# Kernel tuning notes

Hardware: AMD Instinct MI355X
Metric: run time of the kernel (lower is better)

## Reference

```python
import math
import jax, jax.numpy as jnp
import numpy as np

B, S, D = 4, 2048, 1280
H, HD = 16, 80  # num_heads, head_dim
LOG2E = 1.442695041


def setup_inputs() -> dict:
    key = jax.random.key(0)
    ks = jax.random.split(key, 6)
    hidden_states = jax.random.normal(ks[0], (B, S, D), dtype=jnp.float32)
    # additive causal mask: 0 on/below diagonal, large negative above
    causal = jnp.tril(jnp.ones((S, S), dtype=bool))
    attention_mask = jnp.where(causal, 0.0, -1e9).astype(jnp.float32)[None, None, :, :]
    attention_mask = jnp.broadcast_to(attention_mask, (B, 1, S, S))
    scaling = jax.random.normal(ks[1], (HD,), dtype=jnp.float32)
    fan = 1.0 / math.sqrt(D)
    qkv_w = jax.random.normal(ks[2], (3 * H * HD, D), dtype=jnp.float32) * fan
    qkv_b = jax.random.normal(ks[3], (3 * H * HD,), dtype=jnp.float32) * fan
    o_w = jax.random.normal(ks[4], (D, H * HD), dtype=jnp.float32) * (1.0 / math.sqrt(H * HD))
    o_b = jax.random.normal(ks[5], (D,), dtype=jnp.float32) * fan
    return {
        "hidden_states": hidden_states,
        "attention_mask": attention_mask,
        "scaling": scaling,
        "qkv_w": qkv_w,
        "qkv_b": qkv_b,
        "o_w": o_w,
        "o_b": o_b,
    }


def reference(hidden_states, attention_mask, scaling, qkv_w, qkv_b, o_w, o_b):
    b, s, _ = hidden_states.shape
    qkv = hidden_states @ qkv_w.T + qkv_b  # [b, s, 3*H*HD]
    xq, xk, xv = jnp.split(qkv, [H * HD, 2 * H * HD], axis=-1)
    xq = xq.reshape(b, s, H, HD)
    xk = xk.reshape(b, s, H, HD)
    xv = xv.reshape(b, s, H, HD)
    # per-dim query scaling: softplus(scaling) * log2(e) / sqrt(head_dim)
    scale = jax.nn.softplus(scaling) * (LOG2E / math.sqrt(HD))
    xq = xq * scale[None, None, None, :]
    scores = jnp.einsum("bqhd,bkhd->bhqk", xq, xk) + attention_mask  # [b,H,s,s]
    probs = jax.nn.softmax(scores.astype(jnp.float32), axis=-1).astype(xq.dtype)
    out = jnp.einsum("bhqk,bkhd->bqhd", probs, xv).reshape(b, s, H * HD)
    return out @ o_w.T + o_b
```

## Files before the change

kernel.cpp:

```cpp
#include <hip/hip_runtime.h>
#include <math.h>

#define B_ 4
#define S_ 2048
#define D_ 1280
#define H_ 16
#define HD_ 80
#define HHD (H_ * HD_)
#define QKVN (3 * H_ * HD_)

typedef __bf16 bf16x8 __attribute__((ext_vector_type(8)));
typedef __bf16 bf16x4 __attribute__((ext_vector_type(4)));
typedef float  f32x4  __attribute__((ext_vector_type(4)));

__global__ __launch_bounds__(256) void cvt_bf16(
    const float* __restrict__ in, __bf16* __restrict__ out, int n8)
{
    const int i = blockIdx.x * 256 + threadIdx.x;
    if (i < n8) {
        const float4 a = ((const float4*)in)[2 * (size_t)i];
        const float4 b = ((const float4*)in)[2 * (size_t)i + 1];
        bf16x8 v = {(__bf16)a.x, (__bf16)a.y, (__bf16)a.z, (__bf16)a.w,
                    (__bf16)b.x, (__bf16)b.y, (__bf16)b.z, (__bf16)b.w};
        *(bf16x8*)(out + 8 * (size_t)i) = v;
    }
}

__device__ __forceinline__ void async_copy16(const void* g, void* l)
{
    __builtin_amdgcn_global_load_lds(
        (const __attribute__((address_space(1))) unsigned int*)g,
        (__attribute__((address_space(3))) unsigned int*)l, 16, 0, 0);
}

__device__ __forceinline__ void stage128x64(
    const __bf16* __restrict__ src, int K, char* lds, int tid)
{
    const int wave = tid >> 6, lane = tid & 63;
#pragma unroll
    for (int i = 0; i < 4; ++i) {
        const int c = (wave * 4 + i) * 64 + lane;
        const int r = c >> 3;
        const int g = (c & 7) ^ (r & 7);
        async_copy16(src + (size_t)r * K + g * 8, lds + (wave * 4 + i) * 1024);
    }
}

__device__ __forceinline__ bf16x8 frag_ld(const char* lds, int m, int j)
{
    return *(const bf16x8*)(lds + m * 128 + ((j ^ (m & 7)) << 4));
}

__device__ __forceinline__ void mfma_loop(
    const __bf16* __restrict__ A, const __bf16* __restrict__ W, int K,
    char* ldsA, char* ldsB, int tid, f32x4 acc[4][4])
{
    const int wave = tid >> 6;
    const int wm = wave >> 1, wn = wave & 1;
    const int l16 = tid & 15, quad = (tid & 63) >> 4;

#pragma unroll
    for (int mi = 0; mi < 4; ++mi)
#pragma unroll
        for (int ni = 0; ni < 4; ++ni) acc[mi][ni] = (f32x4){0.f, 0.f, 0.f, 0.f};

    for (int k0 = 0; k0 < K; k0 += 64) {
        __syncthreads();
        stage128x64(A + k0, K, ldsA, tid);
        stage128x64(W + k0, K, ldsB, tid);
        __syncthreads();
#pragma unroll
        for (int ks = 0; ks < 2; ++ks) {
            bf16x8 af[4], bfr[4];
#pragma unroll
            for (int mi = 0; mi < 4; ++mi)
                af[mi] = frag_ld(ldsA, wm * 64 + mi * 16 + l16, ks * 4 + quad);
#pragma unroll
            for (int ni = 0; ni < 4; ++ni)
                bfr[ni] = frag_ld(ldsB, wn * 64 + ni * 16 + l16, ks * 4 + quad);
#pragma unroll
            for (int mi = 0; mi < 4; ++mi)
#pragma unroll
                for (int ni = 0; ni < 4; ++ni)
                    acc[mi][ni] = __builtin_amdgcn_mfma_f32_16x16x32_bf16(
                        af[mi], bfr[ni], acc[mi][ni], 0, 0, 0);
        }
    }
}

__global__ __launch_bounds__(256) void gemm_qkv_mfma(
    const __bf16* __restrict__ Ab, const __bf16* __restrict__ Wb,
    const float* __restrict__ bias, const float* __restrict__ scaling,
    __bf16* __restrict__ Qb, __bf16* __restrict__ Kb, __bf16* __restrict__ Vtb)
{
    __shared__ __align__(16) char ldsA[128 * 128];
    __shared__ __align__(16) char ldsB[128 * 128];
    const int tid = threadIdx.x;

    const int flat = blockIdx.x;
    const int xcd = flat & 7;
    const int idx = flat >> 3;
    const int g = idx / 24;
    const int r24 = idx - g * 24;
    const int nn = r24 >> 3;
    const int mm = r24 & 7;
    const int m0 = (xcd * 8 + mm) * 128;
    const int n0 = (g * 3 + nn) * 128;

    f32x4 acc[4][4];
    mfma_loop(Ab + (size_t)m0 * D_, Wb + (size_t)n0 * D_, D_, ldsA, ldsB, tid, acc);

    const int wave = tid >> 6, wm = wave >> 1, wn = wave & 1;
    const int l16 = tid & 15, quad = (tid & 63) >> 4;
    const int sec = n0 / HHD;

    if (sec == 2) {
#pragma unroll
        for (int ni = 0; ni < 4; ++ni) {
            const int col = n0 + wn * 64 + ni * 16 + l16;
            const int cis = col - 2 * HHD;
            const int h = cis / HD_;
            const int d = cis - h * HD_;
            const float bv = bias[col];
#pragma unroll
            for (int mi = 0; mi < 4; ++mi) {
                const int row0 = m0 + wm * 64 + mi * 16 + quad * 4;
                const int bb = row0 >> 11;
                const int s = row0 & (S_ - 1);
                const size_t bh = (size_t)(bb * H_ + h);
                bf16x4 pv = {(__bf16)(acc[mi][ni][0] + bv),
                             (__bf16)(acc[mi][ni][1] + bv),
                             (__bf16)(acc[mi][ni][2] + bv),
                             (__bf16)(acc[mi][ni][3] + bv)};
                *(bf16x4*)(Vtb + (bh * HD_ + d) * S_ + s) = pv;
            }
        }
    } else {
#pragma unroll
        for (int ni = 0; ni < 4; ++ni) {
            const int col = n0 + wn * 64 + ni * 16 + l16;
            const int cis = col - sec * HHD;
            const int h = cis / HD_;
            const int d = cis - h * HD_;
            const float bv = bias[col];
            float qsv = 0.f;
            if (sec == 0)
                qsv = log1pf(expf(scaling[d])) *
                      (1.442695041f * 1.442695041f / 8.944271910f);
#pragma unroll
            for (int mi = 0; mi < 4; ++mi) {
#pragma unroll
                for (int r = 0; r < 4; ++r) {
                    const int row = m0 + wm * 64 + mi * 16 + quad * 4 + r;
                    const int bb = row >> 11;
                    const int s = row & (S_ - 1);
                    const size_t bh = (size_t)(bb * H_ + h);
                    const float v = acc[mi][ni][r] + bv;
                    if (sec == 0) Qb[(bh * S_ + s) * HD_ + d] = (__bf16)(v * qsv);
                    else          Kb[(bh * S_ + s) * HD_ + d] = (__bf16)v;
                }
            }
        }
    }
}

__global__ __launch_bounds__(256) void gemm_o_mfma(
    const __bf16* __restrict__ Ab, const __bf16* __restrict__ Wb,
    const float* __restrict__ bias, float* __restrict__ C)
{
    __shared__ __align__(16) char ldsA[128 * 128];
    __shared__ __align__(16) char ldsB[128 * 128];
    const int tid = threadIdx.x;

    const int flat = blockIdx.x;
    const int xcd = flat & 7;
    const int idx = flat >> 3;
    const int mm = idx / 10;
    const int nn = idx - mm * 10;
    const int m0 = (xcd * 8 + mm) * 128;
    const int n0 = nn * 128;

    f32x4 acc[4][4];
    mfma_loop(Ab + (size_t)m0 * D_, Wb + (size_t)n0 * D_, D_, ldsA, ldsB, tid, acc);

    const int wave = tid >> 6, wm = wave >> 1, wn = wave & 1;
    const int l16 = tid & 15, quad = (tid & 63) >> 4;

#pragma unroll
    for (int ni = 0; ni < 4; ++ni) {
        const int col = n0 + wn * 64 + ni * 16 + l16;
        const float bv = bias[col];
#pragma unroll
        for (int mi = 0; mi < 4; ++mi) {
#pragma unroll
            for (int r = 0; r < 4; ++r) {
                const int row = m0 + wm * 64 + mi * 16 + quad * 4 + r;
                C[(size_t)row * D_ + col] = acc[mi][ni][r] + bv;
            }
        }
    }
}

struct KF8 { bf16x8 f0, f1, f2; };

__device__ __forceinline__ void kload8(
    const __bf16* __restrict__ base, int row, int quad, KF8& kf)
{
    const __bf16* r = base + (size_t)row * HD_;
    kf.f0 = *(const bf16x8*)(r + quad * 8);
    kf.f1 = *(const bf16x8*)(r + 32 + quad * 8);
    bf16x8 z = {};
    if (quad < 2) z = *(const bf16x8*)(r + 64 + quad * 8);
    kf.f2 = z;
}

#define QK3(SREG, KF, QF)                                                      \
    SREG = __builtin_amdgcn_mfma_f32_16x16x32_bf16(KF.f0, QF.f0, SREG, 0, 0, 0); \
    SREG = __builtin_amdgcn_mfma_f32_16x16x32_bf16(KF.f1, QF.f1, SREG, 0, 0, 0); \
    SREG = __builtin_amdgcn_mfma_f32_16x16x32_bf16(KF.f2, QF.f2, SREG, 0, 0, 0);

#define MASK4(SREG, BASE, Q)                                                   \
    _Pragma("unroll")                                                          \
    for (int i = 0; i < 4; ++i)                                                \
        SREG[i] = ((BASE) + quad * 4 + i <= (Q) + l16) ? SREG[i] : -1e30f;

#define ATTN_BODY64(KT)                                                        \
    {                                                                          \
        const int k0 = (KT) * 64;                                              \
        const bool do_lo = ((KT) < nkt_lo);                  \
         \
        const bf16x8 vf00 = *(const bf16x8*)(Vbase + (size_t)( 0 + l16) * S_ + k0 + quad * 8);      \
        const bf16x8 vf01 = *(const bf16x8*)(Vbase + (size_t)( 0 + l16) * S_ + k0 + 32 + quad * 8); \
        const bf16x8 vf10 = *(const bf16x8*)(Vbase + (size_t)(16 + l16) * S_ + k0 + quad * 8);      \
        const bf16x8 vf11 = *(const bf16x8*)(Vbase + (size_t)(16 + l16) * S_ + k0 + 32 + quad * 8); \
        const bf16x8 vf20 = *(const bf16x8*)(Vbase + (size_t)(32 + l16) * S_ + k0 + quad * 8);      \
        const bf16x8 vf21 = *(const bf16x8*)(Vbase + (size_t)(32 + l16) * S_ + k0 + 32 + quad * 8); \
        const bf16x8 vf30 = *(const bf16x8*)(Vbase + (size_t)(48 + l16) * S_ + k0 + quad * 8);      \
        const bf16x8 vf31 = *(const bf16x8*)(Vbase + (size_t)(48 + l16) * S_ + k0 + 32 + quad * 8); \
        const bf16x8 vf40 = *(const bf16x8*)(Vbase + (size_t)(64 + l16) * S_ + k0 + quad * 8);      \
        const bf16x8 vf41 = *(const bf16x8*)(Vbase + (size_t)(64 + l16) * S_ + k0 + 32 + quad * 8); \
                          \
        f32x4 sH0 = (f32x4){0.f,0.f,0.f,0.f}, sH1 = sH0, sH2 = sH0, sH3 = sH0; \
        f32x4 sL0 = sH0, sL1 = sH0, sL2 = sH0, sL3 = sH0;                      \
        __builtin_amdgcn_s_setprio(1);                                         \
        QK3(sH0, kf0, qfH) QK3(sH1, kf1, qfH) QK3(sH2, kf2, qfH) QK3(sH3, kf3, qfH) \
        if (do_lo) {                                                           \
            QK3(sL0, kf0, qfL) QK3(sL1, kf1, qfL)                              \
            QK3(sL2, kf2, qfL) QK3(sL3, kf3, qfL)                              \
        }                                                                      \
        __builtin_amdgcn_s_setprio(0);                                         \
         \
         \
        {                                                                      \
            const int kn = ((KT) + 1 < nkt_hi ? (KT) + 1 : (KT)) * 64;         \
            kload8(Kbase, kn + l16, quad, kf0);                                \
            kload8(Kbase, kn + 16 + l16, quad, kf1);                           \
            kload8(Kbase, kn + 32 + l16, quad, kf2);                           \
            kload8(Kbase, kn + 48 + l16, quad, kf3);                           \
        }                                                                      \
                \
        float aH;                                                              \
        {                                                                      \
            if (k0 + 63 > q_hi) {                                              \
                MASK4(sH0, k0, q_hi)      MASK4(sH1, k0 + 16, q_hi)            \
                MASK4(sH2, k0 + 32, q_hi) MASK4(sH3, k0 + 48, q_hi)            \
            }                                                                  \
            float mA = fmaxf(fmaxf(sH0[0], sH0[1]), fmaxf(sH0[2], sH0[3]));    \
            float mB = fmaxf(fmaxf(sH1[0], sH1[1]), fmaxf(sH1[2], sH1[3]));    \
            float mC = fmaxf(fmaxf(sH2[0], sH2[1]), fmaxf(sH2[2], sH2[3]));    \
            float mD = fmaxf(fmaxf(sH3[0], sH3[1]), fmaxf(sH3[2], sH3[3]));    \
            float mx = fmaxf(fmaxf(mA, mB), fmaxf(mC, mD));                    \
            mx = fmaxf(mx, __shfl_xor(mx, 16));                                \
            mx = fmaxf(mx, __shfl_xor(mx, 32));                                \
            const float mn = fmaxf(mH, mx);                                    \
            aH = exp2f(mH - mn);                                               \
            mH = mn;                                                           \
            float rs = 0.f;                                                    \
            _Pragma("unroll")                                                  \
            for (int i = 0; i < 4; ++i) {                                      \
                const float p0 = exp2f(sH0[i] - mn);                           \
                const float p1 = exp2f(sH1[i] - mn);                           \
                const float p2 = exp2f(sH2[i] - mn);                           \
                const float p3 = exp2f(sH3[i] - mn);                           \
                sH0[i] = p0; sH1[i] = p1; sH2[i] = p2; sH3[i] = p3;            \
                rs += (p0 + p1) + (p2 + p3);                                   \
            }                                                                  \
            lH = lH * aH + rs;                           \
            *(bf16x4*)&Ps[wave][0][l16][0][quad * 4] =                         \
                (bf16x4){(__bf16)sH0[0], (__bf16)sH0[1], (__bf16)sH0[2], (__bf16)sH0[3]}; \
            *(bf16x4*)&Ps[wave][0][l16][0][16 + quad * 4] =                    \
                (bf16x4){(__bf16)sH1[0], (__bf16)sH1[1], (__bf16)sH1[2], (__bf16)sH1[3]}; \
            *(bf16x4*)&Ps[wave][0][l16][1][quad * 4] =                         \
                (bf16x4){(__bf16)sH2[0], (__bf16)sH2[1], (__bf16)sH2[2], (__bf16)sH2[3]}; \
            *(bf16x4*)&Ps[wave][0][l16][1][16 + quad * 4] =                    \
                (bf16x4){(__bf16)sH3[0], (__bf16)sH3[1], (__bf16)sH3[2], (__bf16)sH3[3]}; \
        }                                                                      \
                                          \
        float aL = 1.f;                                                        \
        if (do_lo) {                                                           \
            if (k0 + 63 > q_lo) {                                              \
                MASK4(sL0, k0, q_lo)      MASK4(sL1, k0 + 16, q_lo)            \
                MASK4(sL2, k0 + 32, q_lo) MASK4(sL3, k0 + 48, q_lo)            \
            }                                                                  \
            float mA = fmaxf(fmaxf(sL0[0], sL0[1]), fmaxf(sL0[2], sL0[3]));    \
            float mB = fmaxf(fmaxf(sL1[0], sL1[1]), fmaxf(sL1[2], sL1[3]));    \
            float mC = fmaxf(fmaxf(sL2[0], sL2[1]), fmaxf(sL2[2], sL2[3]));    \
            float mD = fmaxf(fmaxf(sL3[0], sL3[1]), fmaxf(sL3[2], sL3[3]));    \
            float mx = fmaxf(fmaxf(mA, mB), fmaxf(mC, mD));                    \
            mx = fmaxf(mx, __shfl_xor(mx, 16));                                \
            mx = fmaxf(mx, __shfl_xor(mx, 32));                                \
            const float mn = fmaxf(mL, mx);                                    \
            aL = exp2f(mL - mn);                                               \
            mL = mn;                                                           \
            float rs = 0.f;                                                    \
            _Pragma("unroll")                                                  \
            for (int i = 0; i < 4; ++i) {                                      \
                const float p0 = exp2f(sL0[i] - mn);                           \
                const float p1 = exp2f(sL1[i] - mn);                           \
                const float p2 = exp2f(sL2[i] - mn);                           \
                const float p3 = exp2f(sL3[i] - mn);                           \
                sL0[i] = p0; sL1[i] = p1; sL2[i] = p2; sL3[i] = p3;            \
                rs += (p0 + p1) + (p2 + p3);                                   \
            }                                                                  \
            lL = lL * aL + rs;                                                 \
            *(bf16x4*)&Ps[wave][1][l16][0][quad * 4] =                         \
                (bf16x4){(__bf16)sL0[0], (__bf16)sL0[1], (__bf16)sL0[2], (__bf16)sL0[3]}; \
            *(bf16x4*)&Ps[wave][1][l16][0][16 + quad * 4] =                    \
                (bf16x4){(__bf16)sL1[0], (__bf16)sL1[1], (__bf16)sL1[2], (__bf16)sL1[3]}; \
            *(bf16x4*)&Ps[wave][1][l16][1][quad * 4] =                         \
                (bf16x4){(__bf16)sL2[0], (__bf16)sL2[1], (__bf16)sL2[2], (__bf16)sL2[3]}; \
            *(bf16x4*)&Ps[wave][1][l16][1][16 + quad * 4] =                    \
                (bf16x4){(__bf16)sL3[0], (__bf16)sL3[1], (__bf16)sL3[2], (__bf16)sL3[3]}; \
        }                                                                      \
        asm volatile("s_waitcnt lgkmcnt(0)" ::: "memory");                     \
        const bf16x8 pfH0 = *(const bf16x8*)&Ps[wave][0][l16][0][quad * 8];    \
        const bf16x8 pfH1 = *(const bf16x8*)&Ps[wave][0][l16][1][quad * 8];    \
        const bf16x8 pfL0 = *(const bf16x8*)&Ps[wave][1][l16][0][quad * 8];    \
        const bf16x8 pfL1 = *(const bf16x8*)&Ps[wave][1][l16][1][quad * 8];    \
         \
        __builtin_amdgcn_s_setprio(1);                                         \
        {                                                                      \
            f32x4 c0, c1, c2, c3, c4;                                          \
            _Pragma("unroll")                                                  \
            for (int i = 0; i < 4; ++i) {                                      \
                c0[i] = oH0[i] * aH; c1[i] = oH1[i] * aH; c2[i] = oH2[i] * aH; \
                c3[i] = oH3[i] * aH; c4[i] = oH4[i] * aH;                      \
            }                                                                  \
            oH0 = __builtin_amdgcn_mfma_f32_16x16x32_bf16(vf00, pfH0, c0, 0, 0, 0); \
            oH1 = __builtin_amdgcn_mfma_f32_16x16x32_bf16(vf10, pfH0, c1, 0, 0, 0); \
            oH2 = __builtin_amdgcn_mfma_f32_16x16x32_bf16(vf20, pfH0, c2, 0, 0, 0); \
            oH3 = __builtin_amdgcn_mfma_f32_16x16x32_bf16(vf30, pfH0, c3, 0, 0, 0); \
            oH4 = __builtin_amdgcn_mfma_f32_16x16x32_bf16(vf40, pfH0, c4, 0, 0, 0); \
            oH0 = __builtin_amdgcn_mfma_f32_16x16x32_bf16(vf01, pfH1, oH0, 0, 0, 0); \
            oH1 = __builtin_amdgcn_mfma_f32_16x16x32_bf16(vf11, pfH1, oH1, 0, 0, 0); \
            oH2 = __builtin_amdgcn_mfma_f32_16x16x32_bf16(vf21, pfH1, oH2, 0, 0, 0); \
            oH3 = __builtin_amdgcn_mfma_f32_16x16x32_bf16(vf31, pfH1, oH3, 0, 0, 0); \
            oH4 = __builtin_amdgcn_mfma_f32_16x16x32_bf16(vf41, pfH1, oH4, 0, 0, 0); \
        }                                                                      \
        if (do_lo) {                                                           \
            f32x4 c0, c1, c2, c3, c4;                                          \
            _Pragma("unroll")                                                  \
            for (int i = 0; i < 4; ++i) {                                      \
                c0[i] = oL0[i] * aL; c1[i] = oL1[i] * aL; c2[i] = oL2[i] * aL; \
                c3[i] = oL3[i] * aL; c4[i] = oL4[i] * aL;                      \
            }                                                                  \
            oL0 = __builtin_amdgcn_mfma_f32_16x16x32_bf16(vf00, pfL0, c0, 0, 0, 0); \
            oL1 = __builtin_amdgcn_mfma_f32_16x16x32_bf16(vf10, pfL0, c1, 0, 0, 0); \
            oL2 = __builtin_amdgcn_mfma_f32_16x16x32_bf16(vf20, pfL0, c2, 0, 0, 0); \
            oL3 = __builtin_amdgcn_mfma_f32_16x16x32_bf16(vf30, pfL0, c3, 0, 0, 0); \
            oL4 = __builtin_amdgcn_mfma_f32_16x16x32_bf16(vf40, pfL0, c4, 0, 0, 0); \
            oL0 = __builtin_amdgcn_mfma_f32_16x16x32_bf16(vf01, pfL1, oL0, 0, 0, 0); \
            oL1 = __builtin_amdgcn_mfma_f32_16x16x32_bf16(vf11, pfL1, oL1, 0, 0, 0); \
            oL2 = __builtin_amdgcn_mfma_f32_16x16x32_bf16(vf21, pfL1, oL2, 0, 0, 0); \
            oL3 = __builtin_amdgcn_mfma_f32_16x16x32_bf16(vf31, pfL1, oL3, 0, 0, 0); \
            oL4 = __builtin_amdgcn_mfma_f32_16x16x32_bf16(vf41, pfL1, oL4, 0, 0, 0); \
        }                                                                      \
        __builtin_amdgcn_s_setprio(0);                                         \
    }

__global__ __launch_bounds__(256, 2) void attn_v13(
    const __bf16* __restrict__ Qb, const __bf16* __restrict__ Kb,
    const __bf16* __restrict__ Vtb, __bf16* __restrict__ out)
{
    __shared__ __align__(16) __bf16 Ps[4][2][16][2][40];

    const int tid = threadIdx.x;
    const int wave = tid >> 6;
    const int lane = tid & 63;
    const int l16 = lane & 15;
    const int quad = lane >> 4;

    const int flat = blockIdx.x;
    const int c = flat & 7;
    const int slot = flat >> 3;
    const int bhgrp = slot >> 4;
    const int xslot = slot & 15;
    const int bh = bhgrp * 8 + c;
    const int x = (xslot + 5 * bhgrp) & 15;
    const int b = bh >> 4, h = bh & 15;

    const int q_lo = 64 * x + 16 * wave;
    const int q_hi = 64 * (31 - x) + 16 * wave;

    const __bf16* Qbase = Qb + (size_t)bh * S_ * HD_;
    const __bf16* Kbase = Kb + (size_t)bh * S_ * HD_;
    const __bf16* Vbase = Vtb + (size_t)bh * HD_ * S_;

    KF8 qfL, qfH;
    kload8(Qbase, q_lo + l16, quad, qfL);
    kload8(Qbase, q_hi + l16, quad, qfH);

    float mL = -1e30f, lL = 0.f, mH = -1e30f, lH = 0.f;
    f32x4 oH0 = (f32x4){0.f,0.f,0.f,0.f}, oH1 = oH0, oH2 = oH0, oH3 = oH0, oH4 = oH0;
    f32x4 oL0 = oH0, oL1 = oH0, oL2 = oH0, oL3 = oH0, oL4 = oH0;

    const int nkt_lo = (q_lo + 16 + 63) >> 6;
    const int nkt_hi = (q_hi + 16 + 63) >> 6;

    KF8 kf0, kf1, kf2, kf3;
    kload8(Kbase, l16, quad, kf0);
    kload8(Kbase, 16 + l16, quad, kf1);
    kload8(Kbase, 32 + l16, quad, kf2);
    kload8(Kbase, 48 + l16, quad, kf3);

    for (int kt = 0; kt < nkt_hi; ++kt) {
        ATTN_BODY64(kt);
    }

    float lHs = lH + __shfl_xor(lH, 16);
    lHs += __shfl_xor(lHs, 32);
    float lLs = lL + __shfl_xor(lL, 16);
    lLs += __shfl_xor(lLs, 32);
    const float invH = 1.f / lHs;
    const float invL = 1.f / lLs;
    const size_t rowH = ((size_t)b * S_ + q_hi + l16) * HHD + h * HD_ + quad * 4;
    const size_t rowL = ((size_t)b * S_ + q_lo + l16) * HHD + h * HD_ + quad * 4;
    {
        bf16x4 v0 = {(__bf16)(oH0[0]*invH), (__bf16)(oH0[1]*invH), (__bf16)(oH0[2]*invH), (__bf16)(oH0[3]*invH)};
        bf16x4 v1 = {(__bf16)(oH1[0]*invH), (__bf16)(oH1[1]*invH), (__bf16)(oH1[2]*invH), (__bf16)(oH1[3]*invH)};
        bf16x4 v2 = {(__bf16)(oH2[0]*invH), (__bf16)(oH2[1]*invH), (__bf16)(oH2[2]*invH), (__bf16)(oH2[3]*invH)};
        bf16x4 v3 = {(__bf16)(oH3[0]*invH), (__bf16)(oH3[1]*invH), (__bf16)(oH3[2]*invH), (__bf16)(oH3[3]*invH)};
        bf16x4 v4 = {(__bf16)(oH4[0]*invH), (__bf16)(oH4[1]*invH), (__bf16)(oH4[2]*invH), (__bf16)(oH4[3]*invH)};
        *(bf16x4*)(out + rowH)      = v0;
        *(bf16x4*)(out + rowH + 16) = v1;
        *(bf16x4*)(out + rowH + 32) = v2;
        *(bf16x4*)(out + rowH + 48) = v3;
        *(bf16x4*)(out + rowH + 64) = v4;
    }
    {
        bf16x4 v0 = {(__bf16)(oL0[0]*invL), (__bf16)(oL0[1]*invL), (__bf16)(oL0[2]*invL), (__bf16)(oL0[3]*invL)};
        bf16x4 v1 = {(__bf16)(oL1[0]*invL), (__bf16)(oL1[1]*invL), (__bf16)(oL1[2]*invL), (__bf16)(oL1[3]*invL)};
        bf16x4 v2 = {(__bf16)(oL2[0]*invL), (__bf16)(oL2[1]*invL), (__bf16)(oL2[2]*invL), (__bf16)(oL2[3]*invL)};
        bf16x4 v3 = {(__bf16)(oL3[0]*invL), (__bf16)(oL3[1]*invL), (__bf16)(oL3[2]*invL), (__bf16)(oL3[3]*invL)};
        bf16x4 v4 = {(__bf16)(oL4[0]*invL), (__bf16)(oL4[1]*invL), (__bf16)(oL4[2]*invL), (__bf16)(oL4[3]*invL)};
        *(bf16x4*)(out + rowL)      = v0;
        *(bf16x4*)(out + rowL + 16) = v1;
        *(bf16x4*)(out + rowL + 32) = v2;
        *(bf16x4*)(out + rowL + 48) = v3;
        *(bf16x4*)(out + rowL + 64) = v4;
    }
}

extern "C" void kernel_launch(void* const* d_in, const int* in_sizes, int n_in,
                              void* d_out, int out_size, void* d_ws, size_t ws_size,
                              hipStream_t stream)
{
    const float* hidden  = (const float*)d_in[0];
    const float* scaling = (const float*)d_in[2];
    const float* qkv_w   = (const float*)d_in[3];
    const float* qkv_b   = (const float*)d_in[4];
    const float* o_w     = (const float*)d_in[5];
    const float* o_b     = (const float*)d_in[6];
    float* out = (float*)d_out;

    const size_t N_HID = (size_t)B_ * S_ * D_;
    const size_t N_QW  = (size_t)QKVN * D_;
    const size_t N_OW  = (size_t)D_ * D_;
    const size_t NPH   = (size_t)B_ * H_ * S_ * HD_;

    __bf16* Ab    = (__bf16*)d_ws;
    __bf16* Wqb   = Ab + N_HID;
    __bf16* Wob   = Wqb + N_QW;
    __bf16* Qb    = Wob + N_OW;
    __bf16* Kb    = Qb + NPH;
    __bf16* Vtb   = Kb + NPH;
    __bf16* attnb = Vtb + NPH;

    dim3 blk(256);

    cvt_bf16<<<dim3(N_HID / 8 / 256), blk, 0, stream>>>(hidden, Ab, N_HID / 8);
    cvt_bf16<<<dim3(N_QW  / 8 / 256), blk, 0, stream>>>(qkv_w, Wqb, N_QW / 8);
    cvt_bf16<<<dim3(N_OW  / 8 / 256), blk, 0, stream>>>(o_w,   Wob, N_OW / 8);

    gemm_qkv_mfma<<<dim3(QKVN / 128 * (B_ * S_ / 128)), blk, 0, stream>>>(
        Ab, Wqb, qkv_b, scaling, Qb, Kb, Vtb);

    attn_v13<<<dim3(16 * H_ * B_), blk, 0, stream>>>(Qb, Kb, Vtb, attnb);

    gemm_o_mfma<<<dim3(D_ / 128 * (B_ * S_ / 128)), blk, 0, stream>>>(
        attnb, Wob, o_b, out);
}
```

Baseline: 476.6 us.

## Replace QKV GEMM with 256x256-tile, 512-thread double-buffered pipelined kernel

Replaces the 128x128-tile QKV projection GEMM with a 256x256-tile kernel that uses 8 waves. It double-buffers LDS and interleaves async staging of the next K-slice with MFMA work on the current one. Larger tiles cut global and LDS traffic per FLOP, and the staged prefetch hides load latency. In exchange it needs 128KB of LDS and many accumulator registers per block, which limits occupancy. With only 480 blocks there is also a risk of poor wave balance across CUs.

New measurement: 463.2 us. 2.8% less time.

```diff
diff --git a/kernel.cpp b/kernel.cpp
--- a/kernel.cpp
+++ b/kernel.cpp
@@ -88,32 +88,111 @@
     }
 }
 
-__global__ __launch_bounds__(256) void gemm_qkv_mfma(
+__device__ __forceinline__ void stage_half256(
+    const __bf16* __restrict__ src, int K, char* ldsmat, int half, int tid)
+{
+    const int wave = tid >> 6, lane = tid & 63;
+#pragma unroll
+    for (int i = 0; i < 2; ++i) {
+        const int c = (i * 8 + wave) * 64 + lane;
+        const int r = half * 128 + (c >> 3);
+        const int g = (c & 7) ^ (r & 7);
+        async_copy16(src + (size_t)r * K + g * 8,
+                     ldsmat + half * 16384 + (i * 8 + wave) * 1024);
+    }
+}
+
+#define QBAR() do { asm volatile("" ::: "memory");                             \
+                    __builtin_amdgcn_s_barrier();                              \
+                    __builtin_amdgcn_sched_barrier(0); } while (0)
+
+__global__ __launch_bounds__(512, 2) void gemm_qkv_256(
     const __bf16* __restrict__ Ab, const __bf16* __restrict__ Wb,
     const float* __restrict__ bias, const float* __restrict__ scaling,
     __bf16* __restrict__ Qb, __bf16* __restrict__ Kb, __bf16* __restrict__ Vtb)
 {
-    __shared__ __align__(16) char ldsA[128 * 128];
-    __shared__ __align__(16) char ldsB[128 * 128];
+    __shared__ __align__(16) char lds[2][2][32768];
     const int tid = threadIdx.x;
+    const int wave = tid >> 6;
+    const int wm = wave >> 2, wn = wave & 3;
+    const int l16 = tid & 15, quad = (tid & 63) >> 4;
 
     const int flat = blockIdx.x;
     const int xcd = flat & 7;
     const int idx = flat >> 3;
-    const int g = idx / 24;
-    const int r24 = idx - g * 24;
-    const int nn = r24 >> 3;
-    const int mm = r24 & 7;
-    const int m0 = (xcd * 8 + mm) * 128;
-    const int n0 = (g * 3 + nn) * 128;
-
-    f32x4 acc[4][4];
-    mfma_loop(Ab + (size_t)m0 * D_, Wb + (size_t)n0 * D_, D_, ldsA, ldsB, tid, acc);
-
-    const int wave = tid >> 6, wm = wave >> 1, wn = wave & 1;
-    const int l16 = tid & 15, quad = (tid & 63) >> 4;
-    const int sec = n0 / HHD;
-
+    const int m_i = idx & 3, n_g = idx >> 2;
+    const int m0 = (xcd * 4 + m_i) * 256;
+    const int n0 = n_g * 256;
+
+    const __bf16* A = Ab + (size_t)m0 * D_;
+    const __bf16* W = Wb + (size_t)n0 * D_;
+
+    f32x4 acc[8][4];
+#pragma unroll
+    for (int mi = 0; mi < 8; ++mi)
+#pragma unroll
+        for (int ni = 0; ni < 4; ++ni) acc[mi][ni] = (f32x4){0.f, 0.f, 0.f, 0.f};
+
+    stage_half256(A, D_, lds[0][0], 0, tid);
+    stage_half256(A, D_, lds[0][0], 1, tid);
+    stage_half256(W, D_, lds[0][1], 0, tid);
+    stage_half256(W, D_, lds[0][1], 1, tid);
+
+    const int nt = D_ / 64;
+    bf16x8 af[4][2], bfr[2][2];
+
+#define RD_A(MH)                                                               \
+    _Pragma("unroll")                                                          \
+    for (int mi = 0; mi < 4; ++mi)                                             \
+        _Pragma("unroll")                                                      \
+        for (int ks = 0; ks < 2; ++ks)                                         \
+            af[mi][ks] = frag_ld(lA, wm * 128 + (MH) * 64 + mi * 16 + l16,     \
+                                 ks * 4 + quad);
+#define RD_B(NH)                                                               \
+    _Pragma("unroll")                                                          \
+    for (int ni = 0; ni < 2; ++ni)                                             \
+        _Pragma("unroll")                                                      \
+        for (int ks = 0; ks < 2; ++ks)                                         \
+            bfr[ni][ks] = frag_ld(lB, wn * 64 + (NH) * 32 + ni * 16 + l16,     \
+                                  ks * 4 + quad);
+#define MM16(MH, NH)                                                           \
+    __builtin_amdgcn_s_setprio(1);                                             \
+    _Pragma("unroll")                                                          \
+    for (int mi = 0; mi < 4; ++mi)                                             \
+        _Pragma("unroll")                                                      \
+        for (int ni = 0; ni < 2; ++ni) {                                       \
+            acc[(MH)*4+mi][(NH)*2+ni] = __builtin_amdgcn_mfma_f32_16x16x32_bf16( \
+                af[mi][0], bfr[ni][0], acc[(MH)*4+mi][(NH)*2+ni], 0, 0, 0);    \
+            acc[(MH)*4+mi][(NH)*2+ni] = __builtin_amdgcn_mfma_f32_16x16x32_bf16( \
+                af[mi][1], bfr[ni][1], acc[(MH)*4+mi][(NH)*2+ni], 0, 0, 0);    \
+        }                                                                      \
+    __builtin_amdgcn_s_setprio(0);
+
+    for (int t = 0; t < nt; ++t) {
+        const int cur = t & 1;
+        const char* lA = lds[cur][0];
+        const char* lB = lds[cur][1];
+        char* sA = lds[cur ^ 1][0];
+        char* sB = lds[cur ^ 1][1];
+        const int kn = (t + 1 < nt ? t + 1 : t) * 64;
+
+        stage_half256(A + kn, D_, sA, 0, tid);
+        asm volatile("s_waitcnt vmcnt(2)" ::: "memory");
+        QBAR();
+        RD_A(0) RD_B(0) MM16(0, 0)
+        stage_half256(A + kn, D_, sA, 1, tid);
+        RD_B(1) MM16(0, 1)
+        stage_half256(W + kn, D_, sB, 0, tid);
+        RD_A(1) RD_B(0) MM16(1, 0)
+        stage_half256(W + kn, D_, sB, 1, tid);
+        RD_B(1) MM16(1, 1)
+        QBAR();
+    }
+#undef RD_A
+#undef RD_B
+#undef MM16
+
+    const int sec = n_g / 5;
     if (sec == 2) {
 #pragma unroll
         for (int ni = 0; ni < 4; ++ni) {
@@ -123,8 +202,8 @@
             const int d = cis - h * HD_;
             const float bv = bias[col];
 #pragma unroll
-            for (int mi = 0; mi < 4; ++mi) {
-                const int row0 = m0 + wm * 64 + mi * 16 + quad * 4;
+            for (int mi = 0; mi < 8; ++mi) {
+                const int row0 = m0 + wm * 128 + mi * 16 + quad * 4;
                 const int bb = row0 >> 11;
                 const int s = row0 & (S_ - 1);
                 const size_t bh = (size_t)(bb * H_ + h);
@@ -148,10 +227,10 @@
                 qsv = log1pf(expf(scaling[d])) *
                       (1.442695041f * 1.442695041f / 8.944271910f);
 #pragma unroll
-            for (int mi = 0; mi < 4; ++mi) {
+            for (int mi = 0; mi < 8; ++mi) {
 #pragma unroll
                 for (int r = 0; r < 4; ++r) {
-                    const int row = m0 + wm * 64 + mi * 16 + quad * 4 + r;
+                    const int row = m0 + wm * 128 + mi * 16 + quad * 4 + r;
                     const int bb = row >> 11;
                     const int s = row & (S_ - 1);
                     const size_t bh = (size_t)(bb * H_ + h);
@@ -228,7 +307,6 @@
     {                                                                          \
         const int k0 = (KT) * 64;                                              \
         const bool do_lo = ((KT) < nkt_lo);                  \
-         \
         const bf16x8 vf00 = *(const bf16x8*)(Vbase + (size_t)( 0 + l16) * S_ + k0 + quad * 8);      \
         const bf16x8 vf01 = *(const bf16x8*)(Vbase + (size_t)( 0 + l16) * S_ + k0 + 32 + quad * 8); \
         const bf16x8 vf10 = *(const bf16x8*)(Vbase + (size_t)(16 + l16) * S_ + k0 + quad * 8);      \
@@ -239,7 +317,6 @@
         const bf16x8 vf31 = *(const bf16x8*)(Vbase + (size_t)(48 + l16) * S_ + k0 + 32 + quad * 8); \
         const bf16x8 vf40 = *(const bf16x8*)(Vbase + (size_t)(64 + l16) * S_ + k0 + quad * 8);      \
         const bf16x8 vf41 = *(const bf16x8*)(Vbase + (size_t)(64 + l16) * S_ + k0 + 32 + quad * 8); \
-                          \
         f32x4 sH0 = (f32x4){0.f,0.f,0.f,0.f}, sH1 = sH0, sH2 = sH0, sH3 = sH0; \
         f32x4 sL0 = sH0, sL1 = sH0, sL2 = sH0, sL3 = sH0;                      \
         __builtin_amdgcn_s_setprio(1);                                         \
@@ -249,8 +326,6 @@
             QK3(sL2, kf2, qfL) QK3(sL3, kf3, qfL)                              \
         }                                                                      \
         __builtin_amdgcn_s_setprio(0);                                         \
-         \
-         \
         {                                                                      \
             const int kn = ((KT) + 1 < nkt_hi ? (KT) + 1 : (KT)) * 64;         \
             kload8(Kbase, kn + l16, quad, kf0);                                \
@@ -258,7 +333,6 @@
             kload8(Kbase, kn + 32 + l16, quad, kf2);                           \
             kload8(Kbase, kn + 48 + l16, quad, kf3);                           \
         }                                                                      \
-                \
         float aH;                                                              \
         {                                                                      \
             if (k0 + 63 > q_hi) {                                              \
@@ -285,7 +359,7 @@
                 sH0[i] = p0; sH1[i] = p1; sH2[i] = p2; sH3[i] = p3;            \
                 rs += (p0 + p1) + (p2 + p3);                                   \
             }                                                                  \
-            lH = lH * aH + rs;                           \
+            lH = lH * aH + rs;                                                 \
             *(bf16x4*)&Ps[wave][0][l16][0][quad * 4] =                         \
                 (bf16x4){(__bf16)sH0[0], (__bf16)sH0[1], (__bf16)sH0[2], (__bf16)sH0[3]}; \
             *(bf16x4*)&Ps[wave][0][l16][0][16 + quad * 4] =                    \
@@ -295,7 +369,6 @@
             *(bf16x4*)&Ps[wave][0][l16][1][16 + quad * 4] =                    \
                 (bf16x4){(__bf16)sH3[0], (__bf16)sH3[1], (__bf16)sH3[2], (__bf16)sH3[3]}; \
         }                                                                      \
-                                          \
         float aL = 1.f;                                                        \
         if (do_lo) {                                                           \
             if (k0 + 63 > q_lo) {                                              \
@@ -337,7 +410,6 @@
         const bf16x8 pfH1 = *(const bf16x8*)&Ps[wave][0][l16][1][quad * 8];    \
         const bf16x8 pfL0 = *(const bf16x8*)&Ps[wave][1][l16][0][quad * 8];    \
         const bf16x8 pfL1 = *(const bf16x8*)&Ps[wave][1][l16][1][quad * 8];    \
-         \
         __builtin_amdgcn_s_setprio(1);                                         \
         {                                                                      \
             f32x4 c0, c1, c2, c3, c4;                                          \
@@ -492,7 +564,7 @@
     cvt_bf16<<<dim3(N_QW  / 8 / 256), blk, 0, stream>>>(qkv_w, Wqb, N_QW / 8);
     cvt_bf16<<<dim3(N_OW  / 8 / 256), blk, 0, stream>>>(o_w,   Wob, N_OW / 8);
 
-    gemm_qkv_mfma<<<dim3(QKVN / 128 * (B_ * S_ / 128)), blk, 0, stream>>>(
+    gemm_qkv_256<<<dim3(480), dim3(512), 0, stream>>>(
         Ab, Wqb, qkv_b, scaling, Qb, Kb, Vtb);
 
     attn_v13<<<dim3(16 * H_ * B_), blk, 0, stream>>>(Qb, Kb, Vtb, attnb);
```
